# Kernel tuning notes

Measured on AMD Instinct MI355X. Metric: run time of the kernel, lower is better.

The kernel has to match this reference:

```python
import jax, jax.numpy as jnp
import numpy as np

B, D, H, W = 4, 64, 64, 64
S = 64          # number of attention segments
N = 8192        # query pixels
K = 4           # n_refs
HID = 256
D9 = D * 9      # feat_unfold 3x3
IN_DIM = D9 + 2 + 2  # +rel_coord +rel_cell


def setup_inputs() -> dict:
    key = jax.random.key(0)
    ks = jax.random.split(key, 10)
    feat = jax.random.normal(ks[0], (B, D, H, W), jnp.float32)
    attn_sftmx = jax.nn.softmax(jax.random.normal(ks[1], (B, H * W, S), jnp.float32), axis=2)
    coord = jax.random.uniform(ks[2], (B, N, 2), jnp.float32) * 2.0 - 1.0  # [-1,1]
    cell = jnp.full((B, N, 2), 2.0 / 256.0, jnp.float32)  # HR cell size for 256x256 output
    def lin(k, fi, fo):
        return jax.random.normal(k, (fi, fo), jnp.float32) / np.sqrt(fi).astype(np.float32)
    w0 = lin(ks[3], IN_DIM, HID); b0 = jnp.zeros((HID,), jnp.float32)
    w1 = lin(ks[4], HID, HID);    b1 = jnp.zeros((HID,), jnp.float32)
    w2 = lin(ks[5], HID, HID);    b2 = jnp.zeros((HID,), jnp.float32)
    w3 = lin(ks[6], HID, HID);    b3 = jnp.zeros((HID,), jnp.float32)
    w4 = lin(ks[7], HID, 3);      b4 = jnp.zeros((3,), jnp.float32)
    return dict(feat=feat, attn_sftmx=attn_sftmx, coord=coord, cell=cell,
                w0=w0, b0=b0, w1=w1, b1=b1, w2=w2, b2=b2, w3=w3, b3=b3, w4=w4, b4=b4)


def _imnet(x, w0, b0, w1, b1, w2, b2, w3, b3, w4, b4):
    h = jax.nn.relu(x @ w0 + b0)
    h = jax.nn.relu(h @ w1 + b1)
    h = jax.nn.relu(h @ w2 + b2)
    h = jax.nn.relu(h @ w3 + b3)
    return h @ w4 + b4


def reference(feat, attn_sftmx, coord, cell, w0, b0, w1, b1, w2, b2, w3, b3, w4, b4):
    Bn, Dc, h, w = feat.shape
    Nq = coord.shape[1]
    hw = h * w
    # ---- feat_unfold: F.unfold(feat, 3, padding=1) -> (B, D*9, h, w), channel order c*9 + ki*3 + kj
    pad = jnp.pad(feat, ((0, 0), (0, 0), (1, 1), (1, 1)))
    patches = jnp.stack([pad[:, :, ki:ki + h, kj:kj + w]
                         for ki in range(3) for kj in range(3)], axis=2)  # (B,D,9,h,w)
    d9 = Dc * 9
    feat_rows = patches.reshape(Bn, d9, h, w).transpose(0, 2, 3, 1).reshape(Bn, hw, d9)  # (B,hw,D9)
    scale_hw = jnp.array([h, w], jnp.float32)
    rel_cell = cell * scale_hw  # (B,N,2)

    # ================= attention ensemble =================
    pc = (coord + 1.0) / 2.0 * scale_hw
    pc = jnp.clip(pc.astype(jnp.int32), 0, hw - 1)
    pc1d = pc[..., 0] * h + pc[..., 1]  # (B,N)
    segm_idx_whole = jnp.argmax(attn_sftmx, axis=2)  # (B,hw)
    segm_idx = jnp.take_along_axis(segm_idx_whole, pc1d, axis=1)  # (B,N)
    attn_t = attn_sftmx.transpose(0, 2, 1)  # (B,S,hw)
    prob_map = jnp.take_along_axis(attn_t, segm_idx[:, :, None], axis=1)  # (B,N,hw)
    ref_probs, ref_coords = jax.lax.top_k(prob_map, K)  # (B,N,K)
    # Faithful to original: ref_coords (values in [0,hw)) index the FLATTENED (B*hw, D9)
    # feature table, i.e. all batches gather batch-0 rows (source-code behavior).
    ref_feats = feat_rows.reshape(Bn * hw, d9)[ref_coords]  # (B,N,K,D9)
    rrc = ref_coords - pc1d[..., None]  # (B,N,K) int
    rel0 = jnp.floor_divide(rrc, h).astype(jnp.float32) / h
    rel1 = jnp.mod(rrc, h).astype(jnp.float32) / w
    rel = jnp.stack([rel0, rel1], axis=-1)  # (B,N,K,2)
    rc_b = jnp.broadcast_to(rel_cell[:, :, None, :], (Bn, Nq, K, 2))
    inp_attn = jnp.concatenate([ref_feats, rel, rc_b], axis=-1)  # (B,N,K,IN)
    pred_attn = _imnet(inp_attn.reshape(-1, inp_attn.shape[-1]),
                       w0, b0, w1, b1, w2, b2, w3, b3, w4, b4).reshape(Bn, Nq, K, -1)
    wprob = ref_probs / jnp.sum(ref_probs, axis=-1, keepdims=True)
    ret_attn = jnp.sum(pred_attn * wprob[..., None], axis=2)  # (B,N,3)

    # ================= local ensemble =================
    rx, ry = 1.0 / h, 1.0 / w  # 2/h/2, 2/w/2
    eps = 1e-6
    offs = jnp.array([[-1., -1.], [-1., 1.], [1., -1.], [1., 1.]], jnp.float32) \
           * jnp.array([rx, ry], jnp.float32) + eps  # (4,2)
    c = jnp.clip(coord[None] + offs[:, None, None, :], -1 + 1e-6, 1 - 1e-6)  # (4,B,N,2)
    # grid_sample nearest, align_corners=False (grid flipped -> c[...,0] is height)
    iy = jnp.clip(jnp.rint(((c[..., 0] + 1.0) * h - 1.0) / 2.0), 0, h - 1).astype(jnp.int32)
    ix = jnp.clip(jnp.rint(((c[..., 1] + 1.0) * w - 1.0) / 2.0), 0, w - 1).astype(jnp.int32)
    flat = iy * w + ix  # (4,B,N)
    bidx = jnp.arange(Bn)[None, :, None]
    q_feat = feat_rows[bidx, flat]  # (4,B,N,D9)
    qc0 = -1.0 + (2.0 * iy.astype(jnp.float32) + 1.0) / h  # make_coord centers
    qc1 = -1.0 + (2.0 * ix.astype(jnp.float32) + 1.0) / w
    rel_coord = jnp.stack([(coord[None, ..., 0] - qc0) * h,
                           (coord[None, ..., 1] - qc1) * w], axis=-1)  # (4,B,N,2)
    rc_l = jnp.broadcast_to(rel_cell[None], (4, Bn, Nq, 2))
    inp_loc = jnp.concatenate([q_feat, rel_coord, rc_l], axis=-1)  # (4,B,N,IN)
    pred_loc = _imnet(inp_loc.reshape(-1, inp_loc.shape[-1]),
                      w0, b0, w1, b1, w2, b2, w3, b3, w4, b4).reshape(4, Bn, Nq, -1)
    area = jnp.abs(rel_coord[..., 0] * rel_coord[..., 1]) + 1e-9  # (4,B,N)
    tot = jnp.sum(area, axis=0)
    wts = area[::-1] / tot[None]  # area swap 0<->3, 1<->2 == reverse
    ret_local = jnp.sum(pred_loc * wts[..., None], axis=0)  # (B,N,3)

    total = float(K + 4)
    return ret_attn * (K / total) + ret_local * (4.0 / total)
```

## Files before the change

### kernel.cpp

```cpp
#include <hip/hip_runtime.h>
#include <hip/hip_bf16.h>
#include <math.h>
#include <stdint.h>

#define B_ 4
#define D_ 64
#define H_ 64
#define W_ 64
#define S_ 64
#define N_ 8192
#define K_ 4
#define HID_ 256
#define HW_ 4096
#define NQ_ (B_*N_)
#define ROWS_ (NQ_*8)

typedef _Float16 h8   __attribute__((ext_vector_type(8)));
typedef _Float16 h4   __attribute__((ext_vector_type(4)));
typedef float    f32x4 __attribute__((ext_vector_type(4)));

__global__ void fused_prep_kernel(const float* __restrict__ feat,
                                  const float* __restrict__ attn,
                                  const float* __restrict__ w0,
                                  const float* __restrict__ w1,
                                  const float* __restrict__ w2,
                                  const float* __restrict__ w3,
                                  const float* __restrict__ w4,
                                  _Float16* __restrict__ featT,
                                  float* __restrict__ attnT,
                                  _Float16* __restrict__ w0F,
                                  _Float16* __restrict__ wF123,
                                  float* __restrict__ w4T,
                                  float* __restrict__ w0tail,
                                  int* __restrict__ segm)
{
  __shared__ float t[64][65];
  int blk = blockIdx.x;
  int tid = threadIdx.x;

  if (blk < 256) {
    int b = blk >> 6, y = blk & 63;
    for (int p = 0; p < 16; ++p) {
      int c = p * 4 + (tid >> 6), x = tid & 63;
      t[c][x] = feat[(((size_t)b * 64 + c) << 12) + (y << 6) + x];
    }
    __syncthreads();
    for (int p = 0; p < 16; ++p) {
      int x = p * 4 + (tid >> 6), c = tid & 63;
      featT[((((size_t)b * 64 + y) * 64 + x) << 6) + c] = (_Float16)t[c][x];
    }
    return;
  }
  blk -= 256;
  if (blk < 256) {
    int b = blk >> 6, j0 = (blk & 63) << 6;
    for (int idx = tid; idx < 4096; idx += 256) {
      int r = idx >> 6, c = idx & 63;
      t[r][c] = attn[((size_t)(b * 4096 + j0 + r)) * 64 + c];
    }
    __syncthreads();
    for (int idx = tid; idx < 4096; idx += 256) {
      int s = idx >> 6, r = idx & 63;
      attnT[((size_t)(b * 64 + s)) * 4096 + j0 + r] = t[r][s];
    }
    return;
  }
  blk -= 256;
  if (blk < 1351) {
    int i = blk * 256 + tid;
    if (i < 147456) {
      int g = i / 36864, rem = i - g * 36864;
      int ks = rem >> 11, rem2 = rem & 2047;
      int cb = rem2 >> 9, e = rem2 & 511;
      int lane = e >> 3, j = e & 7;
      int n = g * 64 + cb * 16 + (lane & 15);
      int k = ks * 32 + (lane >> 4) * 8 + j;
      int kk = k >> 6, cc = k & 63;
      w0F[i] = (_Float16)w0[(cc * 9 + kk) * 256 + n];
      return;
    }
    i -= 147456;
    if (i < 196608) {
      int l = i >> 16, rem = i & 65535;
      int g = rem >> 14, rem2 = rem & 16383;
      int ks = rem2 >> 11, rem3 = rem2 & 2047;
      int cb = rem3 >> 9, e = rem3 & 511;
      int lane = e >> 3, j = e & 7;
      int n = g * 64 + cb * 16 + (lane & 15);
      int k = ks * 32 + (lane >> 4) * 8 + j;
      const float* w = (l == 0) ? w1 : (l == 1) ? w2 : w3;
      wF123[i] = (_Float16)w[k * 256 + n];
      return;
    }
    i -= 196608;
    if (i < 768) { int j = i / 256, c = i - j * 256; w4T[i] = w4[c * 3 + j]; return; }
    i -= 768;
    if (i < 1024) { int j = i >> 8, n = i & 255; w0tail[i] = w0[(576 + j) * 256 + n]; }
    return;
  }
  blk -= 1351;
  {
    int p = blk * 256 + tid;
    if (p >= B_ * HW_) return;
    const float* a = attn + (size_t)p * S_;
    float best = a[0]; int bi = 0;
    for (int s = 1; s < S_; ++s) { float v = a[s]; if (v > best) { best = v; bi = s; } }
    segm[p] = bi;
  }
}

__global__ void topk_kernel(const float* __restrict__ attnT,
                            int* __restrict__ refc, float* __restrict__ wprob)
{
  int bid = blockIdx.x;
  int tid = threadIdx.x;
  __shared__ float sv[256]; __shared__ int si[256];
  __shared__ float cvs[4]; __shared__ int cis[4];

  const float* col = attnT + (size_t)bid * 4096;
  float tv[4] = { -INFINITY, -INFINITY, -INFINITY, -INFINITY };
  int   ti[4] = { 0x7fffffff, 0x7fffffff, 0x7fffffff, 0x7fffffff };
  for (int j = tid; j < HW_; j += 256) {
    float v = col[j];
    if (v > tv[3]) {
      tv[3] = v; ti[3] = j;
      #pragma unroll
      for (int x = 3; x > 0; --x) {
        if (tv[x] > tv[x-1] || (tv[x] == tv[x-1] && ti[x] < ti[x-1])) {
          float fv = tv[x]; tv[x] = tv[x-1]; tv[x-1] = fv;
          int   fi = ti[x]; ti[x] = ti[x-1]; ti[x-1] = fi;
        }
      }
    }
  }
  int ptr = 0;
  for (int r = 0; r < 4; ++r) {
    sv[tid] = (ptr < 4) ? tv[ptr] : -INFINITY;
    si[tid] = (ptr < 4) ? ti[ptr] : 0x7fffffff;
    __syncthreads();
    for (int o = 128; o; o >>= 1) {
      if (tid < o) {
        float v2 = sv[tid + o]; int i2 = si[tid + o];
        if (v2 > sv[tid] || (v2 == sv[tid] && i2 < si[tid])) { sv[tid] = v2; si[tid] = i2; }
      }
      __syncthreads();
    }
    if (tid == 0) { cvs[r] = sv[0]; cis[r] = si[0]; }
    __syncthreads();
    if (ptr < 4 && ti[ptr] == cis[r]) ptr++;
    __syncthreads();
  }
  if (tid == 0) {
    float ssum = cvs[0] + cvs[1] + cvs[2] + cvs[3];
    for (int k = 0; k < 4; ++k) { refc[bid*4 + k] = cis[k]; wprob[bid*4 + k] = cvs[k] / ssum; }
  }
}

__global__ void meta_kernel(const float* __restrict__ coord, const float* __restrict__ cell,
                            const int* __restrict__ segm, const int* __restrict__ refc,
                            const float* __restrict__ wprob,
                            int* __restrict__ msrc, float4* __restrict__ mt,
                            float* __restrict__ mwgt)
{
  int q = blockIdx.x * 256 + threadIdx.x;
  if (q >= NQ_) return;
  int b = q >> 13;
  float c0 = coord[2*q], c1 = coord[2*q + 1];
  float rc0 = cell[2*q] * 64.0f, rc1 = cell[2*q + 1] * 64.0f;

  float pf0 = (c0 + 1.0f) / 2.0f * 64.0f;
  float pf1 = (c1 + 1.0f) / 2.0f * 64.0f;
  int pc0 = (int)pf0, pc1 = (int)pf1;
  pc0 = min(max(pc0, 0), 4095); pc1 = min(max(pc1, 0), 4095);
  int pc1d = pc0 * 64 + pc1;
  int sg = segm[b * 4096 + min(pc1d, 4095)];
  int base = (b * 64 + sg) * 4;
  #pragma unroll
  for (int k = 0; k < 4; ++k) {
    int rc = refc[base + k];
    int rrc = rc - pc1d;
    float rel0 = (float)(rrc >> 6) * 0.015625f;
    float rel1 = (float)(rrc & 63) * 0.015625f;
    int r = q * 8 + k;
    msrc[r] = rc;
    mt[r] = make_float4(rel0, rel1, rc0, rc1);
    mwgt[r] = 0.5f * wprob[base + k];
  }

  const float sg0[4] = { -1.f, -1.f, 1.f, 1.f };
  const float sg1[4] = { -1.f,  1.f, -1.f, 1.f };
  float area[4], rr0[4], rr1[4]; int srcs[4];
  #pragma unroll
  for (int t = 0; t < 4; ++t) {
    float o0 = sg0[t] * 0.015625f + 1e-6f;
    float o1 = sg1[t] * 0.015625f + 1e-6f;
    float cc0 = fminf(fmaxf(c0 + o0, -1.0f + 1e-6f), 1.0f - 1e-6f);
    float cc1 = fminf(fmaxf(c1 + o1, -1.0f + 1e-6f), 1.0f - 1e-6f);
    float vy = ((cc0 + 1.0f) * 64.0f - 1.0f) / 2.0f;
    float vx = ((cc1 + 1.0f) * 64.0f - 1.0f) / 2.0f;
    float fy = fminf(fmaxf(rintf(vy), 0.0f), 63.0f);
    float fx = fminf(fmaxf(rintf(vx), 0.0f), 63.0f);
    int iy = (int)fy, ix = (int)fx;
    srcs[t] = b * 4096 + iy * 64 + ix;
    float qc0 = -1.0f + (2.0f * (float)iy + 1.0f) / 64.0f;
    float qc1 = -1.0f + (2.0f * (float)ix + 1.0f) / 64.0f;
    float r0 = (c0 - qc0) * 64.0f;
    float r1 = (c1 - qc1) * 64.0f;
    rr0[t] = r0; rr1[t] = r1;
    area[t] = fabsf(r0 * r1) + 1e-9f;
  }
  float tot = area[0] + area[1] + area[2] + area[3];
  #pragma unroll
  for (int t = 0; t < 4; ++t) {
    int r = q * 8 + 4 + t;
    msrc[r] = srcs[t];
    mt[r] = make_float4(rr0[t], rr1[t], rc0, rc1);
    mwgt[r] = 0.5f * area[3 - t] / tot;
  }
}

__launch_bounds__(256, 2)
__global__ void p0_kernel(const _Float16* __restrict__ featT,
                          const _Float16* __restrict__ w0F,
                          _Float16* __restrict__ P0h)
{
  int blk = blockIdx.x;
  int b = blk >> 6, y = blk & 63;
  int tid = threadIdx.x;
  int wave = tid >> 6, lane = tid & 63, quad = lane >> 4, l16 = lane & 15;

  f32x4 acc[4][4];
  #pragma unroll
  for (int i = 0; i < 4; i++)
    #pragma unroll
    for (int j = 0; j < 4; j++) { f32x4 z = {0.f,0.f,0.f,0.f}; acc[i][j] = z; }
  h8 zero8 = {0,0,0,0,0,0,0,0};

  #pragma unroll
  for (int ks = 0; ks < 18; ++ks) {
    int k0 = ks * 32 + quad * 8;
    int kk = k0 >> 6, cc = k0 & 63;
    int di = kk / 3 - 1, dj = kk - (kk / 3) * 3 - 1;
    int yy = y + di;
    h8 afr[4];
    #pragma unroll
    for (int rb = 0; rb < 4; rb++) {
      int xx = rb * 16 + l16 + dj;
      if ((unsigned)yy < 64u && (unsigned)xx < 64u)
        afr[rb] = *(const h8*)(featT + ((((size_t)b * 64 + yy) * 64 + xx) << 6) + cc);
      else
        afr[rb] = zero8;
    }
    h8 bfr[4];
    #pragma unroll
    for (int cb = 0; cb < 4; cb++)
      bfr[cb] = *(const h8*)(w0F + ((((size_t)wave * 18 + ks) * 4 + cb) << 9) + lane * 8);
    #pragma unroll
    for (int rb = 0; rb < 4; rb++)
      #pragma unroll
      for (int cb = 0; cb < 4; cb++)
        acc[rb][cb] = __builtin_amdgcn_mfma_f32_16x16x32_f16(afr[rb], bfr[cb], acc[rb][cb], 0, 0, 0);
  }
  int pixbase = blk * 64;
  #pragma unroll
  for (int rb = 0; rb < 4; rb++)
    #pragma unroll
    for (int cb = 0; cb < 4; cb++)
      #pragma unroll
      for (int i = 0; i < 4; i++) {
        int m = rb * 16 + quad * 4 + i;
        int n = wave * 64 + cb * 16 + l16;
        P0h[((size_t)(pixbase + m) << 8) + n] = (_Float16)acc[rb][cb][i];
      }
}

__launch_bounds__(256, 2)
__global__ void trunk_kernel(const _Float16* __restrict__ P0h,
                             const int* __restrict__ msrc,
                             const float4* __restrict__ mt,
                             const float* __restrict__ mwgt,
                             const float* __restrict__ w0tail,
                             const float* __restrict__ b0,
                             const _Float16* __restrict__ wF123,
                             const float* __restrict__ b1,
                             const float* __restrict__ b2,
                             const float* __restrict__ b3,
                             const float* __restrict__ w4T,
                             const float* __restrict__ b4,
                             float* __restrict__ out)
{
  __shared__ _Float16 hS[128][264];
  __shared__ float mwL[128];
  __shared__ float swL[16];
  __shared__ float partB[16][3][4];

  int tid = threadIdx.x;
  int rowbase = blockIdx.x * 128;
  int wv = tid >> 6;

  if (tid < 128) mwL[tid] = mwgt[rowbase + tid];

  {
    int cg = tid & 63;
    float4 wt0 = ((const float4*)w0tail)[cg];
    float4 wt1 = ((const float4*)w0tail)[64 + cg];
    float4 wt2 = ((const float4*)w0tail)[128 + cg];
    float4 wt3 = ((const float4*)w0tail)[192 + cg];
    float4 bb  = ((const float4*)b0)[cg];
    #pragma unroll 1
    for (int g = 0; g < 4; ++g) {
      int srcs[8]; float4 ts[8];
      #pragma unroll
      for (int i = 0; i < 8; ++i) {
        int r = rowbase + g * 32 + i * 4 + wv;
        srcs[i] = msrc[r];
        ts[i] = mt[r];
      }
      #pragma unroll
      for (int i = 0; i < 8; ++i) {
        int rr = g * 32 + i * 4 + wv;
        float4 t = ts[i];
        h4 pv = *(const h4*)(P0h + ((size_t)srcs[i] << 8) + cg * 4);
        h4 v;
        v[0] = (_Float16)fmaxf((float)pv[0] + t.x*wt0.x + t.y*wt1.x + t.z*wt2.x + t.w*wt3.x + bb.x, 0.0f);
        v[1] = (_Float16)fmaxf((float)pv[1] + t.x*wt0.y + t.y*wt1.y + t.z*wt2.y + t.w*wt3.y + bb.y, 0.0f);
        v[2] = (_Float16)fmaxf((float)pv[2] + t.x*wt0.z + t.y*wt1.z + t.z*wt2.z + t.w*wt3.z + bb.z, 0.0f);
        v[3] = (_Float16)fmaxf((float)pv[3] + t.x*wt0.w + t.y*wt1.w + t.z*wt2.w + t.w*wt3.w + bb.w, 0.0f);
        *(h4*)(&hS[rr][cg * 4]) = v;
      }
    }
  }
  __syncthreads();

  int wave = tid >> 6, lane = tid & 63, quad = lane >> 4, l16 = lane & 15;

  #pragma unroll 1
  for (int l = 0; l < 3; ++l) {
    const _Float16* wL = wF123 + (((size_t)l * 4 + wave) << 14);
    const float* bia = (l == 0) ? b1 : (l == 1) ? b2 : b3;
    f32x4 acc[8][4];
    #pragma unroll
    for (int i = 0; i < 8; i++)
      #pragma unroll
      for (int j = 0; j < 4; j++) { f32x4 z = {0.f,0.f,0.f,0.f}; acc[i][j] = z; }

    h8 bP[2][4];
    #pragma unroll
    for (int cb = 0; cb < 4; cb++) {
      bP[0][cb] = *(const h8*)(wL + (((size_t)0 * 4 + cb) << 9) + lane * 8);
      bP[1][cb] = *(const h8*)(wL + (((size_t)1 * 4 + cb) << 9) + lane * 8);
    }

    #pragma unroll
    for (int ks = 0; ks < 8; ++ks) {
      int cur = ks & 1;
      int k0 = ks * 32 + quad * 8;
      h8 afr[8];
      #pragma unroll
      for (int rb = 0; rb < 8; rb++)
        afr[rb] = *(const h8*)(&hS[rb * 16 + l16][k0]);
      #pragma unroll
      for (int rb = 0; rb < 8; rb++)
        #pragma unroll
        for (int cb = 0; cb < 4; cb++)
          acc[rb][cb] = __builtin_amdgcn_mfma_f32_16x16x32_f16(afr[rb], bP[cur][cb], acc[rb][cb], 0, 0, 0);
      if (ks + 2 < 8) {
        #pragma unroll
        for (int cb = 0; cb < 4; cb++)
          bP[cur][cb] = *(const h8*)(wL + (((size_t)(ks + 2) * 4 + cb) << 9) + lane * 8);
      }
    }
    __syncthreads();
    #pragma unroll
    for (int rb = 0; rb < 8; rb++)
      #pragma unroll
      for (int cb = 0; cb < 4; cb++) {
        int n = wave * 64 + cb * 16 + l16;
        float bv = bia[n];
        #pragma unroll
        for (int i = 0; i < 4; i++) {
          int m = rb * 16 + quad * 4 + i;
          hS[m][n] = (_Float16)fmaxf(acc[rb][cb][i] + bv, 0.0f);
        }
      }
    __syncthreads();
  }

  {
    int q = tid >> 4, cpart = tid & 15;
    float accq[16];
    #pragma unroll
    for (int u = 0; u < 16; ++u) accq[u] = 0.0f;
    float sw = 0.0f;
    #pragma unroll
    for (int j = 0; j < 8; ++j) {
      int row = q * 8 + j;
      float w = mwL[row];
      sw += w;
      h8 a = *(const h8*)(&hS[row][cpart * 16]);
      h8 bq = *(const h8*)(&hS[row][cpart * 16 + 8]);
      #pragma unroll
      for (int u = 0; u < 8; ++u) {
        accq[u]     += w * (float)a[u];
        accq[8 + u] += w * (float)bq[u];
      }
    }
    __syncthreads();
    float* hsF = (float*)&hS[0][0];
    #pragma unroll
    for (int u = 0; u < 16; u += 4)
      *(f32x4*)(hsF + q * 256 + cpart * 16 + u) =
        f32x4{accq[u], accq[u+1], accq[u+2], accq[u+3]};
    if (cpart == 0) swL[q] = sw;
  }
  __syncthreads();
  if (tid < 192) {
    int q = tid / 12, r = tid % 12, j = r >> 2, part = r & 3;
    const float* hsF = (const float*)&hS[0][0];
    const float* hp = hsF + q * 256 + part * 64;
    const float* wp = w4T + j * 256 + part * 64;
    float s = 0.0f;
    #pragma unroll
    for (int u = 0; u < 64; ++u) s += hp[u] * wp[u];
    partB[q][j][part] = s;
  }
  __syncthreads();
  if (tid < 48) {
    int q = tid / 3, j = tid % 3;
    float o = partB[q][j][0] + partB[q][j][1] + partB[q][j][2] + partB[q][j][3]
            + b4[j] * swL[q];
    out[(size_t)(blockIdx.x * 16 + q) * 3 + j] = o;
  }
}

extern "C" void kernel_launch(void* const* d_in, const int* in_sizes, int n_in,
                              void* d_out, int out_size, void* d_ws, size_t ws_size,
                              hipStream_t stream)
{
  const float* feat  = (const float*)d_in[0];
  const float* attn  = (const float*)d_in[1];
  const float* coord = (const float*)d_in[2];
  const float* cell  = (const float*)d_in[3];
  const float* w0 = (const float*)d_in[4];
  const float* b0 = (const float*)d_in[5];
  const float* w1 = (const float*)d_in[6];
  const float* b1 = (const float*)d_in[7];
  const float* w2 = (const float*)d_in[8];
  const float* b2 = (const float*)d_in[9];
  const float* w3 = (const float*)d_in[10];
  const float* b3 = (const float*)d_in[11];
  const float* w4 = (const float*)d_in[12];
  const float* b4 = (const float*)d_in[13];
  float* out = (float*)d_out;

  char* ws = (char*)d_ws;
  size_t off = 0;
  auto alloc = [&](size_t bytes) -> char* {
    char* p = ws + off;
    off += (bytes + 255) & ~(size_t)255;
    return p;
  };
  _Float16* featT = (_Float16*)alloc((size_t)B_ * H_ * W_ * D_ * 2);
  _Float16* w0F   = (_Float16*)alloc((size_t)147456 * 2);
  _Float16* wF123 = (_Float16*)alloc((size_t)196608 * 2);
  float*  w4T   = (float*)alloc((size_t)3 * 256 * 4);
  float*  w0tl  = (float*)alloc((size_t)4 * 256 * 4);
  float*  attnT = (float*)alloc((size_t)B_ * S_ * HW_ * 4);
  int*    segm  = (int*)alloc((size_t)B_ * HW_ * 4);
  int*    refc  = (int*)alloc((size_t)B_ * S_ * K_ * 4);
  float*  wprob = (float*)alloc((size_t)B_ * S_ * K_ * 4);
  _Float16* P0h = (_Float16*)alloc((size_t)B_ * HW_ * 256 * 2);
  int*    msrc  = (int*)alloc((size_t)ROWS_ * 4);
  float4* mtb   = (float4*)alloc((size_t)ROWS_ * 16);
  float*  mwgt  = (float*)alloc((size_t)ROWS_ * 4);
  (void)in_sizes; (void)n_in; (void)out_size; (void)ws_size;

  fused_prep_kernel<<<1927, 256, 0, stream>>>(feat, attn, w0, w1, w2, w3, w4,
                                              featT, attnT, w0F, wF123, w4T, w0tl, segm);
  topk_kernel<<<256, 256, 0, stream>>>(attnT, refc, wprob);
  meta_kernel<<<128, 256, 0, stream>>>(coord, cell, segm, refc, wprob, msrc, mtb, mwgt);
  p0_kernel<<<256, 256, 0, stream>>>(featT, w0F, P0h);
  trunk_kernel<<<2048, 256, 0, stream>>>(P0h, msrc, mtb, mwgt, w0tl, b0, wF123,
                                         b1, b2, b3, w4T, b4, out);
}
```

Baseline: 270.5 us.

## Fuse attention transpose, argmax and top-k into prep; split p0 tiles; rework trunk reduction

Drops the attnT transpose buffer and the separate top-k kernel. Each prep block now loads a 64-row attention chunk into shared memory once and computes both the per-pixel argmax and per-segment partial top-4 candidates, and meta_kernel merges the 64 partials per segment into shared memory before doing the per-query work. This removes a full transpose write/read pass and one launch. It also halves the p0 tile so twice as many blocks run, rewrites the final weighted row reduction so each thread owns one channel, and rotates the w4 dot-product index to avoid LDS bank conflicts. In exchange, every meta block redundantly merges the partials for its batch.

```diff
diff --git a/kernel.cpp b/kernel.cpp
--- a/kernel.cpp
+++ b/kernel.cpp
@@ -27,12 +27,13 @@
                                   const float* __restrict__ w3,
                                   const float* __restrict__ w4,
                                   _Float16* __restrict__ featT,
-                                  float* __restrict__ attnT,
                                   _Float16* __restrict__ w0F,
                                   _Float16* __restrict__ wF123,
                                   float* __restrict__ w4T,
                                   float* __restrict__ w0tail,
-                                  int* __restrict__ segm)
+                                  int* __restrict__ segm,
+                                  float* __restrict__ pv,
+                                  int* __restrict__ pi)
 {
   __shared__ float t[64][65];
   int blk = blockIdx.x;
@@ -48,20 +49,6 @@
     for (int p = 0; p < 16; ++p) {
       int x = p * 4 + (tid >> 6), c = tid & 63;
       featT[((((size_t)b * 64 + y) * 64 + x) << 6) + c] = (_Float16)t[c][x];
-    }
-    return;
-  }
-  blk -= 256;
-  if (blk < 256) {
-    int b = blk >> 6, j0 = (blk & 63) << 6;
-    for (int idx = tid; idx < 4096; idx += 256) {
-      int r = idx >> 6, c = idx & 63;
-      t[r][c] = attn[((size_t)(b * 4096 + j0 + r)) * 64 + c];
-    }
-    __syncthreads();
-    for (int idx = tid; idx < 4096; idx += 256) {
-      int s = idx >> 6, r = idx & 63;
-      attnT[((size_t)(b * 64 + s)) * 4096 + j0 + r] = t[r][s];
     }
     return;
   }
@@ -100,70 +87,77 @@
   }
   blk -= 1351;
   {
-    int p = blk * 256 + tid;
-    if (p >= B_ * HW_) return;
-    const float* a = attn + (size_t)p * S_;
-    float best = a[0]; int bi = 0;
-    for (int s = 1; s < S_; ++s) { float v = a[s]; if (v > best) { best = v; bi = s; } }
-    segm[p] = bi;
+    int b = blk >> 6, chunk = blk & 63;
+    int j0 = chunk * 64;
+    for (int idx = tid; idx < 4096; idx += 256) {
+      int r = idx >> 6, c = idx & 63;
+      t[r][c] = attn[((size_t)(b * 4096 + j0 + r)) * 64 + c];
+    }
+    __syncthreads();
+    if (tid >= 64 && tid < 128) {
+      int r = tid - 64;
+      float best = t[r][0]; int bi = 0;
+      for (int s = 1; s < 64; ++s) { float v = t[r][s]; if (v > best) { best = v; bi = s; } }
+      segm[b * 4096 + j0 + r] = bi;
+    } else if (tid < 64) {
+      int s = tid;
+      float tv[4] = { -INFINITY, -INFINITY, -INFINITY, -INFINITY };
+      int   ti[4] = { 0x7fffffff, 0x7fffffff, 0x7fffffff, 0x7fffffff };
+      for (int r = 0; r < 64; ++r) {
+        float v = t[r][s];
+        if (v > tv[3]) {
+          tv[3] = v; ti[3] = j0 + r;
+          #pragma unroll
+          for (int x = 3; x > 0; --x) {
+            if (tv[x] > tv[x-1] || (tv[x] == tv[x-1] && ti[x] < ti[x-1])) {
+              float fv = tv[x]; tv[x] = tv[x-1]; tv[x-1] = fv;
+              int   fi = ti[x]; ti[x] = ti[x-1]; ti[x-1] = fi;
+            }
+          }
+        }
+      }
+      size_t base = (((size_t)(b * 64 + s)) * 64 + chunk) * 4;
+      #pragma unroll
+      for (int k = 0; k < 4; ++k) { pv[base + k] = tv[k]; pi[base + k] = ti[k]; }
+    }
   }
 }
 
-__global__ void topk_kernel(const float* __restrict__ attnT,
-                            int* __restrict__ refc, float* __restrict__ wprob)
-{
-  int bid = blockIdx.x;
-  int tid = threadIdx.x;
-  __shared__ float sv[256]; __shared__ int si[256];
-  __shared__ float cvs[4]; __shared__ int cis[4];
-
-  const float* col = attnT + (size_t)bid * 4096;
-  float tv[4] = { -INFINITY, -INFINITY, -INFINITY, -INFINITY };
-  int   ti[4] = { 0x7fffffff, 0x7fffffff, 0x7fffffff, 0x7fffffff };
-  for (int j = tid; j < HW_; j += 256) {
-    float v = col[j];
-    if (v > tv[3]) {
-      tv[3] = v; ti[3] = j;
-      #pragma unroll
-      for (int x = 3; x > 0; --x) {
-        if (tv[x] > tv[x-1] || (tv[x] == tv[x-1] && ti[x] < ti[x-1])) {
-          float fv = tv[x]; tv[x] = tv[x-1]; tv[x-1] = fv;
-          int   fi = ti[x]; ti[x] = ti[x-1]; ti[x-1] = fi;
-        }
-      }
-    }
-  }
-  int ptr = 0;
-  for (int r = 0; r < 4; ++r) {
-    sv[tid] = (ptr < 4) ? tv[ptr] : -INFINITY;
-    si[tid] = (ptr < 4) ? ti[ptr] : 0x7fffffff;
-    __syncthreads();
-    for (int o = 128; o; o >>= 1) {
-      if (tid < o) {
-        float v2 = sv[tid + o]; int i2 = si[tid + o];
-        if (v2 > sv[tid] || (v2 == sv[tid] && i2 < si[tid])) { sv[tid] = v2; si[tid] = i2; }
-      }
-      __syncthreads();
-    }
-    if (tid == 0) { cvs[r] = sv[0]; cis[r] = si[0]; }
-    __syncthreads();
-    if (ptr < 4 && ti[ptr] == cis[r]) ptr++;
-    __syncthreads();
-  }
-  if (tid == 0) {
-    float ssum = cvs[0] + cvs[1] + cvs[2] + cvs[3];
-    for (int k = 0; k < 4; ++k) { refc[bid*4 + k] = cis[k]; wprob[bid*4 + k] = cvs[k] / ssum; }
-  }
-}
-
 __global__ void meta_kernel(const float* __restrict__ coord, const float* __restrict__ cell,
-                            const int* __restrict__ segm, const int* __restrict__ refc,
-                            const float* __restrict__ wprob,
+                            const int* __restrict__ segm,
+                            const float* __restrict__ pv, const int* __restrict__ pi,
                             int* __restrict__ msrc, float4* __restrict__ mt,
                             float* __restrict__ mwgt)
 {
-  int q = blockIdx.x * 256 + threadIdx.x;
-  if (q >= NQ_) return;
+  __shared__ int   refcL[64][4];
+  __shared__ float wprobL[64][4];
+  int tid = threadIdx.x;
+  int bb = blockIdx.x >> 5;
+  if (tid < 64) {
+    int s = tid;
+    float tv[4] = { -INFINITY, -INFINITY, -INFINITY, -INFINITY };
+    int   ti[4] = { 0x7fffffff, 0x7fffffff, 0x7fffffff, 0x7fffffff };
+    size_t base = ((size_t)(bb * 64 + s)) * 256;
+    for (int c = 0; c < 256; ++c) {
+      float v = pv[base + c]; int ix = pi[base + c];
+      if (v > tv[3] || (v == tv[3] && ix < ti[3])) {
+        tv[3] = v; ti[3] = ix;
+        #pragma unroll
+        for (int x = 3; x > 0; --x) {
+          if (tv[x] > tv[x-1] || (tv[x] == tv[x-1] && ti[x] < ti[x-1])) {
+            float fv = tv[x]; tv[x] = tv[x-1]; tv[x-1] = fv;
+            int   fi = ti[x]; ti[x] = ti[x-1]; ti[x-1] = fi;
+          }
+        }
+      }
+    }
+    float ssum = tv[0] + tv[1] + tv[2] + tv[3];
+    #pragma unroll
+    for (int k = 0; k < 4; ++k) { refcL[s][k] = ti[k]; wprobL[s][k] = tv[k] / ssum; }
+  }
+  __syncthreads();
+
+  int q = blockIdx.x * 256 + tid;
   int b = q >> 13;
   float c0 = coord[2*q], c1 = coord[2*q + 1];
   float rc0 = cell[2*q] * 64.0f, rc1 = cell[2*q + 1] * 64.0f;
@@ -174,26 +168,25 @@
   pc0 = min(max(pc0, 0), 4095); pc1 = min(max(pc1, 0), 4095);
   int pc1d = pc0 * 64 + pc1;
   int sg = segm[b * 4096 + min(pc1d, 4095)];
-  int base = (b * 64 + sg) * 4;
   #pragma unroll
   for (int k = 0; k < 4; ++k) {
-    int rc = refc[base + k];
+    int rc = refcL[sg][k];
     int rrc = rc - pc1d;
     float rel0 = (float)(rrc >> 6) * 0.015625f;
     float rel1 = (float)(rrc & 63) * 0.015625f;
     int r = q * 8 + k;
     msrc[r] = rc;
     mt[r] = make_float4(rel0, rel1, rc0, rc1);
-    mwgt[r] = 0.5f * wprob[base + k];
+    mwgt[r] = 0.5f * wprobL[sg][k];
   }
 
   const float sg0[4] = { -1.f, -1.f, 1.f, 1.f };
   const float sg1[4] = { -1.f,  1.f, -1.f, 1.f };
   float area[4], rr0[4], rr1[4]; int srcs[4];
   #pragma unroll
-  for (int t = 0; t < 4; ++t) {
-    float o0 = sg0[t] * 0.015625f + 1e-6f;
-    float o1 = sg1[t] * 0.015625f + 1e-6f;
+  for (int tt = 0; tt < 4; ++tt) {
+    float o0 = sg0[tt] * 0.015625f + 1e-6f;
+    float o1 = sg1[tt] * 0.015625f + 1e-6f;
     float cc0 = fminf(fmaxf(c0 + o0, -1.0f + 1e-6f), 1.0f - 1e-6f);
     float cc1 = fminf(fmaxf(c1 + o1, -1.0f + 1e-6f), 1.0f - 1e-6f);
     float vy = ((cc0 + 1.0f) * 64.0f - 1.0f) / 2.0f;
@@ -201,21 +194,21 @@
     float fy = fminf(fmaxf(rintf(vy), 0.0f), 63.0f);
     float fx = fminf(fmaxf(rintf(vx), 0.0f), 63.0f);
     int iy = (int)fy, ix = (int)fx;
-    srcs[t] = b * 4096 + iy * 64 + ix;
+    srcs[tt] = b * 4096 + iy * 64 + ix;
     float qc0 = -1.0f + (2.0f * (float)iy + 1.0f) / 64.0f;
     float qc1 = -1.0f + (2.0f * (float)ix + 1.0f) / 64.0f;
     float r0 = (c0 - qc0) * 64.0f;
     float r1 = (c1 - qc1) * 64.0f;
-    rr0[t] = r0; rr1[t] = r1;
-    area[t] = fabsf(r0 * r1) + 1e-9f;
+    rr0[tt] = r0; rr1[tt] = r1;
+    area[tt] = fabsf(r0 * r1) + 1e-9f;
   }
   float tot = area[0] + area[1] + area[2] + area[3];
   #pragma unroll
-  for (int t = 0; t < 4; ++t) {
-    int r = q * 8 + 4 + t;
-    msrc[r] = srcs[t];
-    mt[r] = make_float4(rr0[t], rr1[t], rc0, rc1);
-    mwgt[r] = 0.5f * area[3 - t] / tot;
+  for (int tt = 0; tt < 4; ++tt) {
+    int r = q * 8 + 4 + tt;
+    msrc[r] = srcs[tt];
+    mt[r] = make_float4(rr0[tt], rr1[tt], rc0, rc1);
+    mwgt[r] = 0.5f * area[3 - tt] / tot;
   }
 }
 
@@ -225,13 +218,13 @@
                           _Float16* __restrict__ P0h)
 {
   int blk = blockIdx.x;
-  int b = blk >> 6, y = blk & 63;
+  int b = blk >> 7, y = (blk >> 1) & 63, hr = blk & 1;
   int tid = threadIdx.x;
   int wave = tid >> 6, lane = tid & 63, quad = lane >> 4, l16 = lane & 15;
 
-  f32x4 acc[4][4];
-  #pragma unroll
-  for (int i = 0; i < 4; i++)
+  f32x4 acc[2][4];
+  #pragma unroll
+  for (int i = 0; i < 2; i++)
     #pragma unroll
     for (int j = 0; j < 4; j++) { f32x4 z = {0.f,0.f,0.f,0.f}; acc[i][j] = z; }
   h8 zero8 = {0,0,0,0,0,0,0,0};
@@ -242,10 +235,10 @@
     int kk = k0 >> 6, cc = k0 & 63;
     int di = kk / 3 - 1, dj = kk - (kk / 3) * 3 - 1;
     int yy = y + di;
-    h8 afr[4];
-    #pragma unroll
-    for (int rb = 0; rb < 4; rb++) {
-      int xx = rb * 16 + l16 + dj;
+    h8 afr[2];
+    #pragma unroll
+    for (int rb = 0; rb < 2; rb++) {
+      int xx = hr * 32 + rb * 16 + l16 + dj;
       if ((unsigned)yy < 64u && (unsigned)xx < 64u)
         afr[rb] = *(const h8*)(featT + ((((size_t)b * 64 + yy) * 64 + xx) << 6) + cc);
       else
@@ -256,14 +249,14 @@
     for (int cb = 0; cb < 4; cb++)
       bfr[cb] = *(const h8*)(w0F + ((((size_t)wave * 18 + ks) * 4 + cb) << 9) + lane * 8);
     #pragma unroll
-    for (int rb = 0; rb < 4; rb++)
+    for (int rb = 0; rb < 2; rb++)
       #pragma unroll
       for (int cb = 0; cb < 4; cb++)
         acc[rb][cb] = __builtin_amdgcn_mfma_f32_16x16x32_f16(afr[rb], bfr[cb], acc[rb][cb], 0, 0, 0);
   }
-  int pixbase = blk * 64;
-  #pragma unroll
-  for (int rb = 0; rb < 4; rb++)
+  int pixbase = b * 4096 + y * 64 + hr * 32;
+  #pragma unroll
+  for (int rb = 0; rb < 2; rb++)
     #pragma unroll
     for (int cb = 0; cb < 4; cb++)
       #pragma unroll
@@ -320,12 +313,12 @@
       for (int i = 0; i < 8; ++i) {
         int rr = g * 32 + i * 4 + wv;
         float4 t = ts[i];
-        h4 pv = *(const h4*)(P0h + ((size_t)srcs[i] << 8) + cg * 4);
+        h4 pvv = *(const h4*)(P0h + ((size_t)srcs[i] << 8) + cg * 4);
         h4 v;
-        v[0] = (_Float16)fmaxf((float)pv[0] + t.x*wt0.x + t.y*wt1.x + t.z*wt2.x + t.w*wt3.x + bb.x, 0.0f);
-        v[1] = (_Float16)fmaxf((float)pv[1] + t.x*wt0.y + t.y*wt1.y + t.z*wt2.y + t.w*wt3.y + bb.y, 0.0f);
-        v[2] = (_Float16)fmaxf((float)pv[2] + t.x*wt0.z + t.y*wt1.z + t.z*wt2.z + t.w*wt3.z + bb.z, 0.0f);
-        v[3] = (_Float16)fmaxf((float)pv[3] + t.x*wt0.w + t.y*wt1.w + t.z*wt2.w + t.w*wt3.w + bb.w, 0.0f);
+        v[0] = (_Float16)fmaxf((float)pvv[0] + t.x*wt0.x + t.y*wt1.x + t.z*wt2.x + t.w*wt3.x + bb.x, 0.0f);
+        v[1] = (_Float16)fmaxf((float)pvv[1] + t.x*wt0.y + t.y*wt1.y + t.z*wt2.y + t.w*wt3.y + bb.y, 0.0f);
+        v[2] = (_Float16)fmaxf((float)pvv[2] + t.x*wt0.z + t.y*wt1.z + t.z*wt2.z + t.w*wt3.z + bb.z, 0.0f);
+        v[3] = (_Float16)fmaxf((float)pvv[3] + t.x*wt0.w + t.y*wt1.w + t.z*wt2.w + t.w*wt3.w + bb.w, 0.0f);
         *(h4*)(&hS[rr][cg * 4]) = v;
       }
     }
@@ -387,31 +380,25 @@
   }
 
   {
-    int q = tid >> 4, cpart = tid & 15;
+    if (tid < 16) {
+      float sw = 0.0f;
+      #pragma unroll
+      for (int j = 0; j < 8; ++j) sw += mwL[tid * 8 + j];
+      swL[tid] = sw;
+    }
+    int c = tid;
     float accq[16];
     #pragma unroll
     for (int u = 0; u < 16; ++u) accq[u] = 0.0f;
-    float sw = 0.0f;
-    #pragma unroll
-    for (int j = 0; j < 8; ++j) {
-      int row = q * 8 + j;
+    #pragma unroll
+    for (int row = 0; row < 128; ++row) {
       float w = mwL[row];
-      sw += w;
-      h8 a = *(const h8*)(&hS[row][cpart * 16]);
-      h8 bq = *(const h8*)(&hS[row][cpart * 16 + 8]);
-      #pragma unroll
-      for (int u = 0; u < 8; ++u) {
-        accq[u]     += w * (float)a[u];
-        accq[8 + u] += w * (float)bq[u];
-      }
+      accq[row >> 3] += w * (float)hS[row][c];
     }
     __syncthreads();
     float* hsF = (float*)&hS[0][0];
     #pragma unroll
-    for (int u = 0; u < 16; u += 4)
-      *(f32x4*)(hsF + q * 256 + cpart * 16 + u) =
-        f32x4{accq[u], accq[u+1], accq[u+2], accq[u+3]};
-    if (cpart == 0) swL[q] = sw;
+    for (int q = 0; q < 16; ++q) hsF[q * 256 + c] = accq[q];
   }
   __syncthreads();
   if (tid < 192) {
@@ -419,9 +406,13 @@
     const float* hsF = (const float*)&hS[0][0];
     const float* hp = hsF + q * 256 + part * 64;
     const float* wp = w4T + j * 256 + part * 64;
+    int u0 = tid & 63;
     float s = 0.0f;
     #pragma unroll
-    for (int u = 0; u < 64; ++u) s += hp[u] * wp[u];
+    for (int u = 0; u < 64; ++u) {
+      int uu = (u0 + u) & 63;
+      s += hp[uu] * wp[uu];
+    }
     partB[q][j][part] = s;
   }
   __syncthreads();
@@ -465,21 +456,20 @@
   _Float16* wF123 = (_Float16*)alloc((size_t)196608 * 2);
   float*  w4T   = (float*)alloc((size_t)3 * 256 * 4);
   float*  w0tl  = (float*)alloc((size_t)4 * 256 * 4);
-  float*  attnT = (float*)alloc((size_t)B_ * S_ * HW_ * 4);
   int*    segm  = (int*)alloc((size_t)B_ * HW_ * 4);
-  int*    refc  = (int*)alloc((size_t)B_ * S_ * K_ * 4);
-  float*  wprob = (float*)alloc((size_t)B_ * S_ * K_ * 4);
+  float*  pv    = (float*)alloc((size_t)B_ * S_ * 64 * 4 * 4);
+  int*    pi    = (int*)alloc((size_t)B_ * S_ * 64 * 4 * 4);
   _Float16* P0h = (_Float16*)alloc((size_t)B_ * HW_ * 256 * 2);
   int*    msrc  = (int*)alloc((size_t)ROWS_ * 4);
   float4* mtb   = (float4*)alloc((size_t)ROWS_ * 16);
   float*  mwgt  = (float*)alloc((size_t)ROWS_ * 4);
   (void)in_sizes; (void)n_in; (void)out_size; (void)ws_size;
 
-  fused_prep_kernel<<<1927, 256, 0, stream>>>(feat, attn, w0, w1, w2, w3, w4,
-                                              featT, attnT, w0F, wF123, w4T, w0tl, segm);
-  topk_kernel<<<256, 256, 0, stream>>>(attnT, refc, wprob);
-  meta_kernel<<<128, 256, 0, stream>>>(coord, cell, segm, refc, wprob, msrc, mtb, mwgt);
-  p0_kernel<<<256, 256, 0, stream>>>(featT, w0F, P0h);
+  fused_prep_kernel<<<1863, 256, 0, stream>>>(feat, attn, w0, w1, w2, w3, w4,
+                                              featT, w0F, wF123, w4T, w0tl,
+                                              segm, pv, pi);
+  meta_kernel<<<128, 256, 0, stream>>>(coord, cell, segm, pv, pi, msrc, mtb, mwgt);
+  p0_kernel<<<512, 256, 0, stream>>>(featT, w0F, P0h);
   trunk_kernel<<<2048, 256, 0, stream>>>(P0h, msrc, mtb, mwgt, w0tl, b0, wF123,
                                          b1, b2, b3, w4T, b4, out);
 }
```

Measured after the change: 291.4 us. 7.7% more time.
